# Kernel tuning notes

Measured on AMD Instinct MI355X. Metric: run time of the kernel, lower is better.

Reference implementation:

```python
import jax, jax.numpy as jnp
import numpy as np

H, W, C = 56, 56, 384
WS, SHIFT, HEADS = 7, 3, 12
HEAD_DIM = C // HEADS
SCALE = HEAD_DIM ** (-0.5)
NWIN = (H // WS) * (W // WS)  # 64 windows per image
NTOK = WS * WS                # 49 tokens per window
EPS = 1e-5


def _gen_mask():
    # static shift-window attention mask, computed with numpy (jit-safe constant)
    img = np.zeros((H, W))
    sl = (slice(0, -WS), slice(-WS, -SHIFT), slice(-SHIFT, None))
    cnt = 0
    for hs in sl:
        for ws in sl:
            img[hs, ws] = cnt
            cnt += 1
    mw = img.reshape(H // WS, WS, W // WS, WS).transpose(0, 2, 1, 3).reshape(-1, NTOK)
    diff = mw[:, None, :] - mw[:, :, None]  # (NWIN, NTOK, NTOK)
    return jnp.asarray(np.where(diff != 0, -100.0, 0.0), dtype=jnp.float32)

ATTN_MASK = _gen_mask()


def _layernorm(x, g, b):
    mu = jnp.mean(x, axis=-1, keepdims=True)
    var = jnp.var(x, axis=-1, keepdims=True)
    return (x - mu) * jax.lax.rsqrt(var + EPS) * g + b


def setup_inputs() -> dict:
    key = jax.random.key(0)
    ks = jax.random.split(key, 6)
    s = 0.02
    return {
        "x": jax.random.normal(ks[0], (16, H * W, C), dtype=jnp.float32),
        "ln1_g": jnp.ones((C,), jnp.float32),
        "ln1_b": jnp.zeros((C,), jnp.float32),
        "qkv_w": jax.random.normal(ks[1], (C, 3 * C), jnp.float32) * s,
        "proj_w": jax.random.normal(ks[2], (C, C), jnp.float32) * s,
        "proj_b": jnp.zeros((C,), jnp.float32),
        "ln2_g": jnp.ones((C,), jnp.float32),
        "ln2_b": jnp.zeros((C,), jnp.float32),
        "fc1_w": jax.random.normal(ks[3], (C, 4 * C), jnp.float32) * s,
        "fc1_b": jnp.zeros((4 * C,), jnp.float32),
        "fc2_w": jax.random.normal(ks[4], (4 * C, C), jnp.float32) * s,
        "fc2_b": jnp.zeros((C,), jnp.float32),
    }


def reference(x, ln1_g, ln1_b, qkv_w, proj_w, proj_b, ln2_g, ln2_b, fc1_w, fc1_b, fc2_w, fc2_b):
    B, N, _ = x.shape
    h = x
    y = _layernorm(x, ln1_g, ln1_b).reshape(B, H, W, C)
    # cyclic shift (note: source never rolls back; we match it)
    y = jnp.roll(y, shift=(-SHIFT, -SHIFT), axis=(1, 2))
    # window partition -> (B*NWIN, NTOK, C)
    y = y.reshape(B, H // WS, WS, W // WS, WS, C).transpose(0, 1, 3, 2, 4, 5)
    y = y.reshape(B * NWIN, NTOK, C)
    # qkv (no bias), split heads
    qkv = (y @ qkv_w).reshape(B * NWIN, NTOK, 3, HEADS, HEAD_DIM)
    qkv = qkv.transpose(2, 0, 3, 1, 4)  # (3, BW, heads, NTOK, hd)
    q, k, v = qkv[0], qkv[1], qkv[2]
    attn = jnp.einsum('whnd,whmd->whnm', q, k) * SCALE  # (BW, heads, NTOK, NTOK)
    attn = attn.reshape(B, NWIN, HEADS, NTOK, NTOK) + ATTN_MASK[None, :, None]
    attn = jax.nn.softmax(attn.reshape(B * NWIN, HEADS, NTOK, NTOK), axis=-1)
    o = jnp.einsum('whnm,whmd->whnd', attn, v)
    o = o.transpose(0, 2, 1, 3).reshape(B * NWIN, NTOK, C)
    o = o @ proj_w + proj_b
    # window reverse -> (B, N, C)
    o = o.reshape(B, H // WS, W // WS, WS, WS, C).transpose(0, 1, 3, 2, 4, 5)
    o = o.reshape(B, N, C)
    x1 = h + o
    # MLP (GELU after both fc1 and fc2, as in source)
    m = _layernorm(x1, ln2_g, ln2_b)
    m = jax.nn.gelu(m @ fc1_w + fc1_b, approximate=False)
    m = jax.nn.gelu(m @ fc2_w + fc2_b, approximate=False)
    return x1 + m
```

## Files before the change

### kernel.cpp

```cpp
#include <hip/hip_runtime.h>
#include <hip/hip_bf16.h>
#include <cstdint>
#include <cstddef>

#define C_DIM   384
#define NIMG    3136
#define MROWS   50176
#define QK_SCALE 0.17677669529663687f

using bf16x8 = __attribute__((ext_vector_type(8))) short;
using f32x4  = __attribute__((ext_vector_type(4))) float;

__device__ __forceinline__ short f2bf(float f) {
  union { float f; uint32_t u; } v; v.f = f;
  uint32_t r = (v.u + 0x7fffu + ((v.u >> 16) & 1u)) >> 16;
  return (short)(uint16_t)r;
}

__device__ __forceinline__ float bf2f(short s) {
  union { uint32_t u; float f; } v; v.u = ((uint32_t)(uint16_t)s) << 16;
  return v.f;
}

__device__ __forceinline__ void async_copy16(const void* g, void* l) {
  __builtin_amdgcn_global_load_lds(
      (const __attribute__((address_space(1))) void*)g,
      (__attribute__((address_space(3))) void*)l, 16, 0, 0);
}

__device__ __forceinline__ float gelu_exact(float x) {
  return 0.5f * x * (1.0f + erff(x * 0.7071067811865475f));
}

__global__ __launch_bounds__(256) void transpose_cast(
    const float* __restrict__ w, short* __restrict__ wt, int K, int N) {
  int idx = blockIdx.x * 256 + threadIdx.x;
  if (idx >= K * N) return;
  int k = idx / N;
  int n = idx - k * N;
  wt[(size_t)n * K + k] = f2bf(w[idx]);
}

template <typename IN>
__global__ __launch_bounds__(256) void ln_kernel(
    const IN* __restrict__ x, const float* __restrict__ g,
    const float* __restrict__ b, short* __restrict__ y, int windowed) {
  int token = blockIdx.x * 4 + (threadIdx.x >> 6);
  int lane = threadIdx.x & 63;
  size_t src;
  if (windowed) {
    int bw = token / 49;
    int tt = token - bw * 49;
    int bb = bw >> 6, w = bw & 63;
    int hs = (w >> 3) * 7 + tt / 7 + 3; if (hs >= 56) hs -= 56;
    int ws = (w & 7) * 7 + (tt % 7) + 3; if (ws >= 56) ws -= 56;
    src = (size_t)(bb * NIMG + hs * 56 + ws) * C_DIM;
  } else {
    src = (size_t)token * C_DIM;
  }
  const IN* xr = x + src;
  float v[6];
  float s = 0.f;
#pragma unroll
  for (int i = 0; i < 6; ++i) {
    if constexpr (sizeof(IN) == 4) v[i] = (float)xr[lane + i * 64];
    else v[i] = bf2f((short)xr[lane + i * 64]);
    s += v[i];
  }
#pragma unroll
  for (int m = 1; m < 64; m <<= 1) s += __shfl_xor(s, m);
  float mu = s * (1.0f / 384.0f);
  float var = 0.f;
#pragma unroll
  for (int i = 0; i < 6; ++i) { float d = v[i] - mu; var += d * d; }
#pragma unroll
  for (int m = 1; m < 64; m <<= 1) var += __shfl_xor(var, m);
  float rstd = rsqrtf(var * (1.0f / 384.0f) + 1e-5f);
  short* yr = y + (size_t)token * C_DIM;
#pragma unroll
  for (int i = 0; i < 6; ++i) {
    int c = lane + i * 64;
    yr[c] = f2bf((v[i] - mu) * rstd * g[c] + b[c]);
  }
}

template <int EPI>
__global__ __launch_bounds__(256, 2) void gemm_kernel(
    const short* __restrict__ A, const short* __restrict__ Bt,
    void* __restrict__ Out, const float* __restrict__ bias,
    const void* __restrict__ resid, int M, int N, int K, int nby) {
  __shared__ __align__(16) short lds[2][128 * 64 * 2];
  const int t = threadIdx.x;
  const int wave = t >> 6, lane = t & 63;
  const int lrow = lane & 15, quad = lane >> 4;
  const int wm = wave & 1, wn = wave >> 1;

  const int wg = (int)blockIdx.x;
  const int swz = (wg & 7) * ((int)gridDim.x >> 3) + (wg >> 3);
  const int mb = swz / nby;
  const int nb = swz - mb * nby;
  const int m0 = mb * 128, n0 = nb * 128;

  f32x4 acc[4][4] = {};

  const int srow = t >> 3;
  const int spos = t & 7;

  const int nt = K >> 6;

  auto stage = [&](int buf, int k0) {
    short* la = &lds[buf][0];
    short* lb = la + 128 * 64;
#pragma unroll
    for (int i = 0; i < 4; ++i) {
      int row = i * 32 + srow;
      int ca = spos ^ (row & 7);
      async_copy16(A + (size_t)(m0 + row) * K + k0 + ca * 8,
                   la + (i * 32 + wave * 8) * 64);
      async_copy16(Bt + (size_t)(n0 + row) * K + k0 + ca * 8,
                   lb + (i * 32 + wave * 8) * 64);
    }
  };

  stage(0, 0);

  for (int kt = 0; kt < nt; ++kt) {
    __builtin_amdgcn_sched_barrier(0);
    if (kt + 1 < nt) {
      stage((kt + 1) & 1, (kt + 1) * 64);
      asm volatile("s_waitcnt vmcnt(8)" ::: "memory");
    } else {
      asm volatile("s_waitcnt vmcnt(0)" ::: "memory");
    }
    __builtin_amdgcn_s_barrier();
    __builtin_amdgcn_sched_barrier(0);

    short* ldsA = &lds[kt & 1][0];
    short* ldsB = ldsA + 128 * 64;
#pragma unroll
    for (int ks = 0; ks < 2; ++ks) {
      const int cb = ks * 4;
      bf16x8 af[4], bfr[4];
#pragma unroll
      for (int i = 0; i < 4; ++i) {
        int ra = wm * 64 + i * 16 + lrow;
        af[i] = *(const bf16x8*)(ldsA + ra * 64 + (((cb + quad) ^ (ra & 7)) * 8));
        int rb = wn * 64 + i * 16 + lrow;
        bfr[i] = *(const bf16x8*)(ldsB + rb * 64 + (((cb + quad) ^ (rb & 7)) * 8));
      }
      __builtin_amdgcn_s_setprio(1);
#pragma unroll
      for (int i = 0; i < 4; ++i)
#pragma unroll
        for (int j = 0; j < 4; ++j)
          acc[i][j] = __builtin_amdgcn_mfma_f32_16x16x32_bf16(af[i], bfr[j],
                                                              acc[i][j], 0, 0, 0);
      __builtin_amdgcn_s_setprio(0);
    }
    __builtin_amdgcn_sched_barrier(0);
    __builtin_amdgcn_s_barrier();
  }

#pragma unroll
  for (int i = 0; i < 4; ++i) {
#pragma unroll
    for (int r = 0; r < 4; ++r) {
      int row = m0 + wm * 64 + i * 16 + quad * 4 + r;
      if (EPI == 1) {
        int bw = row / 49;
        int tt = row - bw * 49;
        int bb = bw >> 6, w = bw & 63;
        int nimg = ((w >> 3) * 7 + tt / 7) * 56 + (w & 7) * 7 + (tt % 7);
        size_t obase = ((size_t)(bb * NIMG + nimg)) * C_DIM;
#pragma unroll
        for (int j = 0; j < 4; ++j) {
          int col = n0 + wn * 64 + j * 16 + lrow;
          size_t oi = obase + col;
          ((short*)Out)[oi] =
              f2bf(acc[i][j][r] + bias[col] + ((const float*)resid)[oi]);
        }
      } else {
#pragma unroll
        for (int j = 0; j < 4; ++j) {
          int col = n0 + wn * 64 + j * 16 + lrow;
          float v = acc[i][j][r];
          if (EPI == 0) {
            ((short*)Out)[(size_t)row * N + col] = f2bf(v);
          } else if (EPI == 2) {
            ((short*)Out)[(size_t)row * N + col] = f2bf(gelu_exact(v + bias[col]));
          } else {
            size_t oi = (size_t)row * C_DIM + col;
            ((float*)Out)[oi] =
                bf2f(((const short*)resid)[oi]) + gelu_exact(v + bias[col]);
          }
        }
      }
    }
  }
}

__global__ __launch_bounds__(256) void attn_kernel(
    const short* __restrict__ qkv, short* __restrict__ o) {
  __shared__ __align__(16) short plds[4][64 * 72];
  const int wavei = threadIdx.x >> 6;
  const int lane = threadIdx.x & 63;
  const int gw = blockIdx.x * 4 + wavei;
  const int bw = gw / 12;
  const int h = gw - bw * 12;
  const int w = bw & 63;
  const int lrow = lane & 15, quad = lane >> 4;
  const short* base = qkv + (size_t)bw * 49 * 1152 + h * 32;

  bf16x8 qf[4], kf[4];
#pragma unroll
  for (int i = 0; i < 4; ++i) {
    int tq = i * 16 + lrow;
    const short* p = base + (size_t)tq * 1152 + quad * 8;
    qf[i] = *(const bf16x8*)p;
    kf[i] = *(const bf16x8*)(p + 384);
  }
  f32x4 sa[4][4] = {};
#pragma unroll
  for (int i = 0; i < 4; ++i)
#pragma unroll
    for (int j = 0; j < 4; ++j)
      sa[i][j] = __builtin_amdgcn_mfma_f32_16x16x32_bf16(qf[i], kf[j], sa[i][j], 0, 0, 0);

  int tl = lane < 49 ? lane : 0;
  int rr = tl / 7, cc = tl - rr * 7;
  int hs = (w >> 3) * 7 + rr;
  int ws = (w & 7) * 7 + cc;
  int id = (hs < 49 ? 0 : (hs < 53 ? 3 : 6)) + (ws < 49 ? 0 : (ws < 53 ? 1 : 2));

  int idn[4], idm[4][4];
#pragma unroll
  for (int j = 0; j < 4; ++j) idn[j] = __shfl(id, j * 16 + lrow);
#pragma unroll
  for (int i = 0; i < 4; ++i)
#pragma unroll
    for (int r = 0; r < 4; ++r) idm[i][r] = __shfl(id, i * 16 + quad * 4 + r);

#pragma unroll
  for (int i = 0; i < 4; ++i)
#pragma unroll
    for (int j = 0; j < 4; ++j)
#pragma unroll
      for (int r = 0; r < 4; ++r) {
        float v = sa[i][j][r] * QK_SCALE + (idm[i][r] == idn[j] ? 0.f : -100.f);
        sa[i][j][r] = (j * 16 + lrow < 49) ? v : -1e30f;
      }

#pragma unroll
  for (int i = 0; i < 4; ++i)
#pragma unroll
    for (int r = 0; r < 4; ++r) {
      float mx = -1e30f;
#pragma unroll
      for (int j = 0; j < 4; ++j) mx = fmaxf(mx, sa[i][j][r]);
#pragma unroll
      for (int m = 1; m < 16; m <<= 1) mx = fmaxf(mx, __shfl_xor(mx, m));
      float sum = 0.f;
#pragma unroll
      for (int j = 0; j < 4; ++j) {
        float e = exp2f((sa[i][j][r] - mx) * 1.44269504f);
        sa[i][j][r] = e;
        sum += e;
      }
#pragma unroll
      for (int m = 1; m < 16; m <<= 1) sum += __shfl_xor(sum, m);
      float inv = 1.0f / sum;
#pragma unroll
      for (int j = 0; j < 4; ++j) sa[i][j][r] *= inv;
    }

  short* pw = plds[wavei];
#pragma unroll
  for (int i = 0; i < 4; ++i)
#pragma unroll
    for (int r = 0; r < 4; ++r)
#pragma unroll
      for (int j = 0; j < 4; ++j)
        pw[(i * 16 + quad * 4 + r) * 72 + j * 16 + lrow] = f2bf(sa[i][j][r]);

  f32x4 oa[4][2] = {};
#pragma unroll
  for (int kk = 0; kk < 2; ++kk) {
    bf16x8 vf[2];
#pragma unroll
    for (int j2 = 0; j2 < 2; ++j2) {
#pragma unroll
      for (int jj = 0; jj < 8; ++jj) {
        int n = kk * 32 + quad * 8 + jj;
        vf[j2][jj] = (n < 49)
            ? base[768 + (size_t)n * 1152 + j2 * 16 + lrow]
            : (short)0;
      }
    }
#pragma unroll
    for (int i = 0; i < 4; ++i) {
      bf16x8 pf = *(const bf16x8*)(pw + (i * 16 + lrow) * 72 + kk * 32 + quad * 8);
#pragma unroll
      for (int j2 = 0; j2 < 2; ++j2)
        oa[i][j2] = __builtin_amdgcn_mfma_f32_16x16x32_bf16(pf, vf[j2], oa[i][j2], 0, 0, 0);
    }
  }

#pragma unroll
  for (int i = 0; i < 4; ++i)
#pragma unroll
    for (int j2 = 0; j2 < 2; ++j2)
#pragma unroll
      for (int r = 0; r < 4; ++r) {
        int m = i * 16 + quad * 4 + r;
        if (m < 49)
          o[((size_t)bw * 49 + m) * 384 + h * 32 + j2 * 16 + lrow] = f2bf(oa[i][j2][r]);
      }
}

extern "C" void kernel_launch(void* const* d_in, const int* in_sizes, int n_in,
                              void* d_out, int out_size, void* d_ws, size_t ws_size,
                              hipStream_t stream) {
  const float* x      = (const float*)d_in[0];
  const float* ln1_g  = (const float*)d_in[1];
  const float* ln1_b  = (const float*)d_in[2];
  const float* qkv_w  = (const float*)d_in[3];
  const float* proj_w = (const float*)d_in[4];
  const float* proj_b = (const float*)d_in[5];
  const float* ln2_g  = (const float*)d_in[6];
  const float* ln2_b  = (const float*)d_in[7];
  const float* fc1_w  = (const float*)d_in[8];
  const float* fc1_b  = (const float*)d_in[9];
  const float* fc2_w  = (const float*)d_in[10];
  const float* fc2_b  = (const float*)d_in[11];
  float* out = (float*)d_out;

  char* ws = (char*)d_ws;
  auto alloc = [&](size_t bytes) {
    char* p = ws;
    ws += (bytes + 255) & ~(size_t)255;
    return p;
  };
  short* qkv_wT  = (short*)alloc((size_t)1152 * 384 * 2);
  short* proj_wT = (short*)alloc((size_t)384 * 384 * 2);
  short* fc1_wT  = (short*)alloc((size_t)1536 * 384 * 2);
  short* fc2_wT  = (short*)alloc((size_t)384 * 1536 * 2);
  short* bufA    = (short*)alloc((size_t)MROWS * 384 * 2);
  short* x1      = (short*)alloc((size_t)MROWS * 384 * 2);
  short* bufB    = (short*)alloc((size_t)MROWS * 1536 * 2);

  transpose_cast<<<(384 * 1152) / 256, 256, 0, stream>>>(qkv_w, qkv_wT, 384, 1152);
  transpose_cast<<<(384 * 384) / 256, 256, 0, stream>>>(proj_w, proj_wT, 384, 384);
  transpose_cast<<<(384 * 1536) / 256, 256, 0, stream>>>(fc1_w, fc1_wT, 384, 1536);
  transpose_cast<<<(1536 * 384) / 256, 256, 0, stream>>>(fc2_w, fc2_wT, 1536, 384);

  ln_kernel<float><<<MROWS / 4, 256, 0, stream>>>(x, ln1_g, ln1_b, bufA, 1);

  gemm_kernel<0><<<392 * 9, 256, 0, stream>>>(bufA, qkv_wT, bufB, nullptr,
                                              nullptr, MROWS, 1152, 384, 9);

  attn_kernel<<<3072, 256, 0, stream>>>(bufB, bufA);

  gemm_kernel<1><<<392 * 3, 256, 0, stream>>>(bufA, proj_wT, x1, proj_b,
                                              x, MROWS, 384, 384, 3);

  ln_kernel<short><<<MROWS / 4, 256, 0, stream>>>(x1, ln2_g, ln2_b, bufA, 0);

  gemm_kernel<2><<<392 * 12, 256, 0, stream>>>(bufA, fc1_wT, bufB, fc1_b,
                                               nullptr, MROWS, 1536, 384, 12);

  gemm_kernel<3><<<392 * 3, 256, 0, stream>>>(bufB, fc2_wT, out, fc2_b,
                                              x1, MROWS, 384, 1536, 3);
}
```

Before: 572.7 us.

## Add tanh-form GELU, single-buffer high-occupancy GEMM, triple-buffered fc2 GEMM

Exact erf GELU is replaced by a tanh-style approximation built from exp2 and a hardware reciprocal, which cuts transcendental cost in the fc1 and fc2 epilogues. The main GEMM becomes single-buffered with synchronous barriers and a launch bound allowing 4 blocks per CU, trading software pipelining for occupancy on the K=384 GEMMs. A new triple-buffered GEMM with K-step 32 handles the K=1536 fc2 layer. The GELU approximation changes numerics slightly, and the non-pipelined GEMM may expose load latency.

After: 517.1 us. 1.11x faster.

```diff
diff --git a/kernel.cpp b/kernel.cpp
--- a/kernel.cpp
+++ b/kernel.cpp
@@ -28,8 +28,12 @@
       (__attribute__((address_space(3))) void*)l, 16, 0, 0);
 }
 
-__device__ __forceinline__ float gelu_exact(float x) {
-  return 0.5f * x * (1.0f + erff(x * 0.7071067811865475f));
+__device__ __forceinline__ float gelu_fast(float x) {
+  float x2 = x * x;
+  float u = fmaf(0.0356774081f, x2, 0.7978845608f);
+  float e = exp2f(x * u * 2.8853900818f);
+  float r = __builtin_amdgcn_rcpf(e + 1.0f);
+  return fmaf(-x, r, x);
 }
 
 __global__ __launch_bounds__(256) void transpose_cast(
@@ -85,82 +89,9 @@
 }
 
 template <int EPI>
-__global__ __launch_bounds__(256, 2) void gemm_kernel(
-    const short* __restrict__ A, const short* __restrict__ Bt,
-    void* __restrict__ Out, const float* __restrict__ bias,
-    const void* __restrict__ resid, int M, int N, int K, int nby) {
-  __shared__ __align__(16) short lds[2][128 * 64 * 2];
-  const int t = threadIdx.x;
-  const int wave = t >> 6, lane = t & 63;
-  const int lrow = lane & 15, quad = lane >> 4;
-  const int wm = wave & 1, wn = wave >> 1;
-
-  const int wg = (int)blockIdx.x;
-  const int swz = (wg & 7) * ((int)gridDim.x >> 3) + (wg >> 3);
-  const int mb = swz / nby;
-  const int nb = swz - mb * nby;
-  const int m0 = mb * 128, n0 = nb * 128;
-
-  f32x4 acc[4][4] = {};
-
-  const int srow = t >> 3;
-  const int spos = t & 7;
-
-  const int nt = K >> 6;
-
-  auto stage = [&](int buf, int k0) {
-    short* la = &lds[buf][0];
-    short* lb = la + 128 * 64;
-#pragma unroll
-    for (int i = 0; i < 4; ++i) {
-      int row = i * 32 + srow;
-      int ca = spos ^ (row & 7);
-      async_copy16(A + (size_t)(m0 + row) * K + k0 + ca * 8,
-                   la + (i * 32 + wave * 8) * 64);
-      async_copy16(Bt + (size_t)(n0 + row) * K + k0 + ca * 8,
-                   lb + (i * 32 + wave * 8) * 64);
-    }
-  };
-
-  stage(0, 0);
-
-  for (int kt = 0; kt < nt; ++kt) {
-    __builtin_amdgcn_sched_barrier(0);
-    if (kt + 1 < nt) {
-      stage((kt + 1) & 1, (kt + 1) * 64);
-      asm volatile("s_waitcnt vmcnt(8)" ::: "memory");
-    } else {
-      asm volatile("s_waitcnt vmcnt(0)" ::: "memory");
-    }
-    __builtin_amdgcn_s_barrier();
-    __builtin_amdgcn_sched_barrier(0);
-
-    short* ldsA = &lds[kt & 1][0];
-    short* ldsB = ldsA + 128 * 64;
-#pragma unroll
-    for (int ks = 0; ks < 2; ++ks) {
-      const int cb = ks * 4;
-      bf16x8 af[4], bfr[4];
-#pragma unroll
-      for (int i = 0; i < 4; ++i) {
-        int ra = wm * 64 + i * 16 + lrow;
-        af[i] = *(const bf16x8*)(ldsA + ra * 64 + (((cb + quad) ^ (ra & 7)) * 8));
-        int rb = wn * 64 + i * 16 + lrow;
-        bfr[i] = *(const bf16x8*)(ldsB + rb * 64 + (((cb + quad) ^ (rb & 7)) * 8));
-      }
-      __builtin_amdgcn_s_setprio(1);
-#pragma unroll
-      for (int i = 0; i < 4; ++i)
-#pragma unroll
-        for (int j = 0; j < 4; ++j)
-          acc[i][j] = __builtin_amdgcn_mfma_f32_16x16x32_bf16(af[i], bfr[j],
-                                                              acc[i][j], 0, 0, 0);
-      __builtin_amdgcn_s_setprio(0);
-    }
-    __builtin_amdgcn_sched_barrier(0);
-    __builtin_amdgcn_s_barrier();
-  }
-
+__device__ __forceinline__ void gemm_epilogue(
+    f32x4 (&acc)[4][4], void* Out, const float* bias, const void* resid,
+    int N, int m0, int n0, int wm, int wn, int lrow, int quad) {
 #pragma unroll
   for (int i = 0; i < 4; ++i) {
 #pragma unroll
@@ -187,16 +118,157 @@
           if (EPI == 0) {
             ((short*)Out)[(size_t)row * N + col] = f2bf(v);
           } else if (EPI == 2) {
-            ((short*)Out)[(size_t)row * N + col] = f2bf(gelu_exact(v + bias[col]));
+            ((short*)Out)[(size_t)row * N + col] = f2bf(gelu_fast(v + bias[col]));
           } else {
             size_t oi = (size_t)row * C_DIM + col;
             ((float*)Out)[oi] =
-                bf2f(((const short*)resid)[oi]) + gelu_exact(v + bias[col]);
+                bf2f(((const short*)resid)[oi]) + gelu_fast(v + bias[col]);
           }
         }
       }
     }
   }
+}
+
+__device__ __forceinline__ void grid_decode(int nby, int& m0, int& n0) {
+  const int wg = (int)blockIdx.x;
+  const int swz = (wg & 7) * ((int)gridDim.x >> 3) + (wg >> 3);
+  const int mb = swz / nby;
+  const int nb = swz - mb * nby;
+  m0 = mb * 128;
+  n0 = nb * 128;
+}
+
+template <int EPI>
+__global__ __launch_bounds__(256, 4) void gemm_kernel(
+    const short* __restrict__ A, const short* __restrict__ Bt,
+    void* __restrict__ Out, const float* __restrict__ bias,
+    const void* __restrict__ resid, int M, int N, int K, int nby) {
+  __shared__ __align__(16) short lds[128 * 64 * 2];
+  const int t = threadIdx.x;
+  const int wave = t >> 6, lane = t & 63;
+  const int lrow = lane & 15, quad = lane >> 4;
+  const int wm = wave & 1, wn = wave >> 1;
+  int m0, n0;
+  grid_decode(nby, m0, n0);
+
+  f32x4 acc[4][4] = {};
+  const int srow = t >> 3;
+  const int spos = t & 7;
+  const int nt = K >> 6;
+  short* ldsA = lds;
+  short* ldsB = lds + 128 * 64;
+
+  for (int kt = 0; kt < nt; ++kt) {
+    int k0 = kt * 64;
+    __syncthreads();
+#pragma unroll
+    for (int i = 0; i < 4; ++i) {
+      int row = i * 32 + srow;
+      int ca = spos ^ (row & 7);
+      async_copy16(A + (size_t)(m0 + row) * K + k0 + ca * 8,
+                   ldsA + (i * 32 + wave * 8) * 64);
+      async_copy16(Bt + (size_t)(n0 + row) * K + k0 + ca * 8,
+                   ldsB + (i * 32 + wave * 8) * 64);
+    }
+    __syncthreads();
+#pragma unroll
+    for (int ks = 0; ks < 2; ++ks) {
+      const int cb = ks * 4;
+      bf16x8 af[4], bfr[4];
+#pragma unroll
+      for (int i = 0; i < 4; ++i) {
+        int ra = wm * 64 + i * 16 + lrow;
+        af[i] = *(const bf16x8*)(ldsA + ra * 64 + (((cb + quad) ^ (ra & 7)) * 8));
+        int rb = wn * 64 + i * 16 + lrow;
+        bfr[i] = *(const bf16x8*)(ldsB + rb * 64 + (((cb + quad) ^ (rb & 7)) * 8));
+      }
+#pragma unroll
+      for (int i = 0; i < 4; ++i)
+#pragma unroll
+        for (int j = 0; j < 4; ++j)
+          acc[i][j] = __builtin_amdgcn_mfma_f32_16x16x32_bf16(af[i], bfr[j],
+                                                              acc[i][j], 0, 0, 0);
+    }
+  }
+  gemm_epilogue<EPI>(acc, Out, bias, resid, N, m0, n0, wm, wn, lrow, quad);
+}
+
+template <int EPI>
+__global__ __launch_bounds__(256, 3) void gemm_pipe_kernel(
+    const short* __restrict__ A, const short* __restrict__ Bt,
+    void* __restrict__ Out, const float* __restrict__ bias,
+    const void* __restrict__ resid, int M, int N, int K, int nby) {
+  __shared__ __align__(16) short lds[3][128 * 32 * 2];
+  const int t = threadIdx.x;
+  const int wave = t >> 6, lane = t & 63;
+  const int lrow = lane & 15, quad = lane >> 4;
+  const int wm = wave & 1, wn = wave >> 1;
+  int m0, n0;
+  grid_decode(nby, m0, n0);
+
+  f32x4 acc[4][4] = {};
+  const int srow = t >> 2;
+  const int spos = t & 3;
+  const int nt = K >> 5;
+
+  auto stage = [&](int buf, int k0) {
+    short* la = &lds[buf][0];
+    short* lb = la + 128 * 32;
+#pragma unroll
+    for (int i = 0; i < 2; ++i) {
+      int row = i * 64 + srow;
+      int ca = spos ^ (row & 3);
+      async_copy16(A + (size_t)(m0 + row) * K + k0 + ca * 8,
+                   la + (i * 64 + wave * 16) * 32);
+      async_copy16(Bt + (size_t)(n0 + row) * K + k0 + ca * 8,
+                   lb + (i * 64 + wave * 16) * 32);
+    }
+  };
+
+  auto compute = [&](int buf) {
+    short* ldsA = &lds[buf][0];
+    short* ldsB = ldsA + 128 * 32;
+    bf16x8 af[4], bfr[4];
+#pragma unroll
+    for (int i = 0; i < 4; ++i) {
+      int ra = wm * 64 + i * 16 + lrow;
+      af[i] = *(const bf16x8*)(ldsA + ra * 32 + ((quad ^ (ra & 3)) * 8));
+      int rb = wn * 64 + i * 16 + lrow;
+      bfr[i] = *(const bf16x8*)(ldsB + rb * 32 + ((quad ^ (rb & 3)) * 8));
+    }
+    __builtin_amdgcn_s_setprio(1);
+#pragma unroll
+    for (int i = 0; i < 4; ++i)
+#pragma unroll
+      for (int j = 0; j < 4; ++j)
+        acc[i][j] = __builtin_amdgcn_mfma_f32_16x16x32_bf16(af[i], bfr[j],
+                                                            acc[i][j], 0, 0, 0);
+    __builtin_amdgcn_s_setprio(0);
+  };
+
+  stage(0, 0);
+  stage(1, 32);
+  int cbuf = 0, sbuf = 2;
+  for (int kt = 0; kt < nt; ++kt) {
+    __builtin_amdgcn_sched_barrier(0);
+    if (kt + 2 < nt) {
+      stage(sbuf, (kt + 2) * 32);
+      asm volatile("s_waitcnt vmcnt(8)" ::: "memory");
+    } else if (kt + 1 < nt) {
+      asm volatile("s_waitcnt vmcnt(4)" ::: "memory");
+    } else {
+      asm volatile("s_waitcnt vmcnt(0)" ::: "memory");
+    }
+    __builtin_amdgcn_s_barrier();
+    __builtin_amdgcn_sched_barrier(0);
+    compute(cbuf);
+    __builtin_amdgcn_sched_barrier(0);
+    __builtin_amdgcn_s_barrier();
+    cbuf = (cbuf == 2) ? 0 : cbuf + 1;
+    sbuf = (sbuf == 2) ? 0 : sbuf + 1;
+  }
+  gemm_epilogue<EPI>(acc, Out, bias, resid, N, m0, n0, wm, wn, lrow, quad);
 }
 
 __global__ __launch_bounds__(256) void attn_kernel(
@@ -368,6 +440,6 @@
   gemm_kernel<2><<<392 * 12, 256, 0, stream>>>(bufA, fc1_wT, bufB, fc1_b,
                                                nullptr, MROWS, 1536, 384, 12);
 
-  gemm_kernel<3><<<392 * 3, 256, 0, stream>>>(bufB, fc2_wT, out, fc2_b,
-                                              x1, MROWS, 384, 1536, 3);
-}
+  gemm_pipe_kernel<3><<<392 * 3, 256, 0, stream>>>(bufB, fc2_wT, out, fc2_b,
+                                                   x1, MROWS, 384, 1536, 3);
+}
```
